# Optimization experiments

Measured on AMD Instinct MI355X. Metric: run time of the kernel, lower is better.

The kernel has to match this reference:

```python
import jax, jax.numpy as jnp
import numpy as np

N_HIDDEN = 32
RANK = 6
SV_DECAY_GAMMA = 0.3
LEAK_ALPHA = 0.1
INPUT_DIM = 64
OUTPUT_DIM = 32


def setup_inputs() -> dict:
    key = jax.random.key(0)
    ks = jax.random.split(key, 8)
    B, T = 256, 2048
    inputs = jax.random.normal(ks[0], (B, T, INPUT_DIM), dtype=jnp.float32)
    # parameters (match torch init scales)
    m = jax.random.normal(ks[1], (N_HIDDEN, 1), dtype=jnp.float32) * 0.1
    n = jax.random.normal(ks[2], (N_HIDDEN, 1), dtype=jnp.float32) * 0.1
    M = jax.random.normal(ks[3], (N_HIDDEN, RANK), dtype=jnp.float32) * 0.1
    Nmat = jax.random.normal(ks[4], (N_HIDDEN, RANK), dtype=jnp.float32) * 0.1
    # singular-value-decay scaling of M, N (as in _initialize_with_sv_decay)
    target_sv = jnp.exp(-SV_DECAY_GAMMA * jnp.arange(RANK, dtype=jnp.float32))
    target_sv = target_sv / target_sv.sum() * RANK
    sqrt_sv = jnp.sqrt(target_sv)
    M = M * sqrt_sv[None, :]
    Nmat = Nmat * sqrt_sv[None, :]
    bias = jnp.zeros((N_HIDDEN,), dtype=jnp.float32)
    # W_in: Linear(input_dim, N, bias=False) -> weight [N, input_dim]
    lim_in = 1.0 / np.sqrt(INPUT_DIM)
    W_in = jax.random.uniform(ks[5], (N_HIDDEN, INPUT_DIM), minval=-lim_in, maxval=lim_in, dtype=jnp.float32)
    lim_out = 1.0 / np.sqrt(N_HIDDEN)
    W_out = jax.random.uniform(ks[6], (OUTPUT_DIM, N_HIDDEN), minval=-lim_out, maxval=lim_out, dtype=jnp.float32)
    b_out = jax.random.uniform(ks[7], (OUTPUT_DIM,), minval=-lim_out, maxval=lim_out, dtype=jnp.float32)
    return {"inputs": inputs, "W_in": W_in, "m": m, "n": n, "M": M,
            "Nmat": Nmat, "bias": bias, "W_out": W_out, "b_out": b_out}


def reference(inputs, W_in, m, n, M, Nmat, bias, W_out, b_out):
    # h_{t+1} = (1-a) h_t + a * tanh(W_rec h_t + W_in u_t + b); y_t = W_out h_t + b_out
    B, T, _ = inputs.shape
    alpha = LEAK_ALPHA
    # W_rec = m n^T + M N^T (time-invariant; torch recomputes per step, same math)
    W_rec = m @ n.T + M @ Nmat.T                         # [N, N]
    x_proj = jnp.einsum('bti,ni->btn', inputs, W_in)     # [B, T, N]
    h0 = jnp.zeros((B, N_HIDDEN), dtype=inputs.dtype)

    def step(h, x_t):
        pre = h @ W_rec.T + x_t + bias
        h_new = (1.0 - alpha) * h + alpha * jnp.tanh(pre)
        return h_new, h_new

    h_final, hs = jax.lax.scan(step, h0, jnp.swapaxes(x_proj, 0, 1))  # hs: [T, B, N]
    outputs = jnp.einsum('tbn,on->bto', hs, W_out) + b_out            # [B, T, O]
    return outputs, h_final
```

## Files before the change

### kernel.cpp

```cpp
#include <hip/hip_runtime.h>

#define RNN_B 256
#define RNN_T 2048
#define RNN_IN 64
#define RNN_N 32
#define RNN_O 32
#define RNN_R 6
#define RNN_ALPHA 0.1f
#define KSCALE 2.8853900817779268f

__global__ __launch_bounds__(256) void k_xproj(
    const float* __restrict__ u, const float* __restrict__ W_in,
    const float* __restrict__ bias, float* __restrict__ xp)
{
    const int tid = blockIdx.x * 256 + threadIdx.x;
    const float4* __restrict__ u4 =
        reinterpret_cast<const float4*>(u) + (size_t)tid * (RNN_IN / 4);
    float acc[RNN_N];
    #pragma unroll
    for (int n = 0; n < RNN_N; ++n) acc[n] = bias[n];
    #pragma unroll
    for (int q = 0; q < RNN_IN / 4; ++q) {
        const float4 v = u4[q];
        #pragma unroll
        for (int n = 0; n < RNN_N; ++n) {
            const float* wr = W_in + n * RNN_IN + 4 * q;
            acc[n] = fmaf(wr[0], v.x, acc[n]);
            acc[n] = fmaf(wr[1], v.y, acc[n]);
            acc[n] = fmaf(wr[2], v.z, acc[n]);
            acc[n] = fmaf(wr[3], v.w, acc[n]);
        }
    }
    float4* __restrict__ o4 =
        reinterpret_cast<float4*>(xp) + (size_t)tid * (RNN_N / 4);
    #pragma unroll
    for (int q = 0; q < RNN_N / 4; ++q)
        o4[q] = make_float4(KSCALE * acc[4*q+0], KSCALE * acc[4*q+1],
                            KSCALE * acc[4*q+2], KSCALE * acc[4*q+3]);
}

template <int CTRL>
__device__ __forceinline__ float dpp_add(float v) {
    int t = __builtin_amdgcn_update_dpp(0, __float_as_int(v), CTRL, 0xf, 0xf, true);
    return v + __int_as_float(t);
}

__device__ __forceinline__ float xhalf_sum(float v) {
#if __has_builtin(__builtin_amdgcn_permlane32_swap)
    typedef int v2i __attribute__((ext_vector_type(2)));
    v2i r = __builtin_amdgcn_permlane32_swap(__float_as_int(v),
                                             __float_as_int(v), false, false);
    return __int_as_float(r.x) + __int_as_float(r.y);
#else
    return v + __shfl_xor(v, 32, 64);
#endif
}

__device__ __forceinline__ float fast_exp2(float x) {
#if __has_builtin(__builtin_amdgcn_exp2f)
    return __builtin_amdgcn_exp2f(x);
#else
    return __expf(x * 0.6931471805599453f);
#endif
}
__device__ __forceinline__ float fast_rcp(float x) {
#if __has_builtin(__builtin_amdgcn_rcpf)
    return __builtin_amdgcn_rcpf(x);
#else
    return __frcp_rn(x);
#endif
}

__global__ __launch_bounds__(64, 1) void k_recur(
    const float* __restrict__ m, const float* __restrict__ nvec,
    const float* __restrict__ Mmat, const float* __restrict__ Nmat,
    const float* __restrict__ xp,
    float* __restrict__ hout,
    float* __restrict__ hfin)
{
    const int b    = blockIdx.x;
    const int lane = threadIdx.x;
    const int k    = lane & 15;
    const int iA   = 2 * k;
    const int iB   = 2 * k + 1;
    const int half = (lane >> 5) & 1;

    float cnA[4], cnB[4], cmA[4], cmB[4];
    #pragma unroll
    for (int j = 0; j < 4; ++j) {
        const int r = 4 * half + j;
        if (r == 0) {
            cnA[j] = nvec[iA];              cnB[j] = nvec[iB];
            cmA[j] = KSCALE * m[iA];        cmB[j] = KSCALE * m[iB];
        } else if (r <= RNN_R) {
            cnA[j] = Nmat[iA*RNN_R + (r-1)];          cnB[j] = Nmat[iB*RNN_R + (r-1)];
            cmA[j] = KSCALE * Mmat[iA*RNN_R + (r-1)]; cmB[j] = KSCALE * Mmat[iB*RNN_R + (r-1)];
        } else {
            cnA[j] = 0.f; cnB[j] = 0.f; cmA[j] = 0.f; cmB[j] = 0.f;
        }
    }
    const float xmask = (half == 0) ? 1.0f : 0.0f;

    const float2* __restrict__ x2 =
        reinterpret_cast<const float2*>(xp + (size_t)b * (RNN_T * RNN_N)) + k;
    float2* __restrict__ h2 =
        reinterpret_cast<float2*>(hout + (size_t)b * (RNN_T * RNN_N));

    float hA = 0.0f, hB = 0.0f;

    const int PF = 8;
    float2 xr[PF];
    #pragma unroll
    for (int i = 0; i < PF; ++i) xr[i] = x2[i * (RNN_N / 2)];

    #pragma unroll 8
    for (int t = 0; t < RNN_T; ++t) {
        const float xA = xr[0].x, xB = xr[0].y;
        #pragma unroll
        for (int i = 0; i < PF - 1; ++i) xr[i] = xr[i + 1];
        xr[PF - 1] = x2[(t + PF) * (RNN_N / 2)];

        float s0 = fmaf(hB, cnB[0], hA * cnA[0]);
        float s1 = fmaf(hB, cnB[1], hA * cnA[1]);
        float s2 = fmaf(hB, cnB[2], hA * cnA[2]);
        float s3 = fmaf(hB, cnB[3], hA * cnA[3]);
        s0 = dpp_add<0xB1>(s0);  s1 = dpp_add<0xB1>(s1);
        s2 = dpp_add<0xB1>(s2);  s3 = dpp_add<0xB1>(s3);
        s0 = dpp_add<0x4E>(s0);  s1 = dpp_add<0x4E>(s1);
        s2 = dpp_add<0x4E>(s2);  s3 = dpp_add<0x4E>(s3);
        s0 = dpp_add<0x141>(s0); s1 = dpp_add<0x141>(s1);
        s2 = dpp_add<0x141>(s2); s3 = dpp_add<0x141>(s3);
        s0 = dpp_add<0x140>(s0); s1 = dpp_add<0x140>(s1);
        s2 = dpp_add<0x140>(s2); s3 = dpp_add<0x140>(s3);

        float tA = fmaf(cmA[0], s0, fmaf(cmA[1], s1, xA * xmask));
        float tB = fmaf(cmB[0], s0, fmaf(cmB[1], s1, xB * xmask));
        float uA = fmaf(cmA[2], s2, cmA[3] * s3);
        float uB = fmaf(cmB[2], s2, cmB[3] * s3);
        const float zA = xhalf_sum(tA + uA);
        const float zB = xhalf_sum(tB + uB);

        const float eA = fast_exp2(zA), eB = fast_exp2(zB);
        const float gA = fmaf(1.0f - RNN_ALPHA, hA, RNN_ALPHA);
        const float gB = fmaf(1.0f - RNN_ALPHA, hB, RNN_ALPHA);
        hA = fmaf(-2.0f * RNN_ALPHA, fast_rcp(eA + 1.0f), gA);
        hB = fmaf(-2.0f * RNN_ALPHA, fast_rcp(eB + 1.0f), gB);

        if (lane < 16) h2[t * (RNN_N / 2) + lane] = make_float2(hA, hB);
    }
    if (lane < 16)
        reinterpret_cast<float2*>(hfin + (size_t)b * RNN_N)[lane] =
            make_float2(hA, hB);
}

__global__ __launch_bounds__(256) void k_out(
    const float* __restrict__ W_out, const float* __restrict__ b_out,
    const float* __restrict__ hsrc, float* __restrict__ ydst)
{
    const int tid = blockIdx.x * 256 + threadIdx.x;
    const float4* __restrict__ p4 =
        reinterpret_cast<const float4*>(hsrc) + (size_t)tid * (RNN_N / 4);
    float4* __restrict__ q4 =
        reinterpret_cast<float4*>(ydst) + (size_t)tid * (RNN_N / 4);
    float y[RNN_O];
    #pragma unroll
    for (int o = 0; o < RNN_O; ++o) y[o] = b_out[o];
    #pragma unroll
    for (int q = 0; q < RNN_N / 4; ++q) {
        const float4 v = p4[q];
        #pragma unroll
        for (int o = 0; o < RNN_O; ++o) {
            const float* wr = W_out + o * RNN_N + 4 * q;
            y[o] = fmaf(wr[0], v.x, y[o]);
            y[o] = fmaf(wr[1], v.y, y[o]);
            y[o] = fmaf(wr[2], v.z, y[o]);
            y[o] = fmaf(wr[3], v.w, y[o]);
        }
    }
    #pragma unroll
    for (int q = 0; q < RNN_N / 4; ++q)
        q4[q] = make_float4(y[4*q+0], y[4*q+1], y[4*q+2], y[4*q+3]);
}

extern "C" void kernel_launch(void* const* d_in, const int* in_sizes, int n_in,
                              void* d_out, int out_size, void* d_ws, size_t ws_size,
                              hipStream_t stream)
{
    const float* u     = (const float*)d_in[0];
    const float* W_in  = (const float*)d_in[1];
    const float* m     = (const float*)d_in[2];
    const float* nvec  = (const float*)d_in[3];
    const float* Mmat  = (const float*)d_in[4];
    const float* Nmat  = (const float*)d_in[5];
    const float* bias  = (const float*)d_in[6];
    const float* W_out = (const float*)d_in[7];
    const float* b_out = (const float*)d_in[8];
    float* out = (float*)d_out;

    float* hfin = out + (size_t)RNN_B * RNN_T * RNN_N;

    const size_t hbytes = (size_t)RNN_B * RNN_T * RNN_N * sizeof(float);
    float* hbuf = (ws_size >= hbytes) ? (float*)d_ws : out;

    k_xproj<<<(RNN_B * RNN_T) / 256, 256, 0, stream>>>(u, W_in, bias, out);
    k_recur<<<RNN_B, 64, 0, stream>>>(m, nvec, Mmat, Nmat, out, hbuf, hfin);
    k_out  <<<(RNN_B * RNN_T) / 256, 256, 0, stream>>>(W_out, b_out, hbuf, out);
}
```

Baseline: 608.4 us.

## Remap recurrence lanes to one hidden element each with staged cross-lane reductions

Changes the recurrent kernel's lane mapping so that each lane owns a single hidden element instead of a pair. Lanes are split by element parity and by rank group. The rank projections are now reduced with DPP within 16 lanes, then a permlane32 swap, and the output contribution with a permlane16 swap. This halves the per-lane exp/rcp and FMA work, and the prefetch buffer becomes a rotating slot instead of a shifted array. The cost is an extra cross-lane swap stage on the serial per-timestep dependency chain, and stores become scalar.

```diff
diff --git a/kernel.cpp b/kernel.cpp
--- a/kernel.cpp
+++ b/kernel.cpp
@@ -44,8 +44,15 @@
     int t = __builtin_amdgcn_update_dpp(0, __float_as_int(v), CTRL, 0xf, 0xf, true);
     return v + __int_as_float(t);
 }
-
-__device__ __forceinline__ float xhalf_sum(float v) {
+__device__ __forceinline__ float sum16(float v) {
+    v = dpp_add<0xB1>(v);
+    v = dpp_add<0x4E>(v);
+    v = dpp_add<0x141>(v);
+    v = dpp_add<0x140>(v);
+    return v;
+}
+
+__device__ __forceinline__ float xsum32(float v) {
 #if __has_builtin(__builtin_amdgcn_permlane32_swap)
     typedef int v2i __attribute__((ext_vector_type(2)));
     v2i r = __builtin_amdgcn_permlane32_swap(__float_as_int(v),
@@ -53,6 +60,16 @@
     return __int_as_float(r.x) + __int_as_float(r.y);
 #else
     return v + __shfl_xor(v, 32, 64);
+#endif
+}
+__device__ __forceinline__ float xsum16(float v) {
+#if __has_builtin(__builtin_amdgcn_permlane16_swap)
+    typedef int v2i __attribute__((ext_vector_type(2)));
+    v2i r = __builtin_amdgcn_permlane16_swap(__float_as_int(v),
+                                             __float_as_int(v), false, false);
+    return __int_as_float(r.x) + __int_as_float(r.y);
+#else
+    return v + __shfl_xor(v, 16, 64);
 #endif
 }
 
@@ -81,49 +98,42 @@
     const int b    = blockIdx.x;
     const int lane = threadIdx.x;
     const int k    = lane & 15;
-    const int iA   = 2 * k;
-    const int iB   = 2 * k + 1;
-    const int half = (lane >> 5) & 1;
-
-    float cnA[4], cnB[4], cmA[4], cmB[4];
+    const int q    = (lane >> 4) & 1;
+    const int p    = lane >> 5;
+    const int e    = 2 * k + p;
+
+    float cn[4], cm[4];
     #pragma unroll
     for (int j = 0; j < 4; ++j) {
-        const int r = 4 * half + j;
-        if (r == 0) {
-            cnA[j] = nvec[iA];              cnB[j] = nvec[iB];
-            cmA[j] = KSCALE * m[iA];        cmB[j] = KSCALE * m[iB];
-        } else if (r <= RNN_R) {
-            cnA[j] = Nmat[iA*RNN_R + (r-1)];          cnB[j] = Nmat[iB*RNN_R + (r-1)];
-            cmA[j] = KSCALE * Mmat[iA*RNN_R + (r-1)]; cmB[j] = KSCALE * Mmat[iB*RNN_R + (r-1)];
-        } else {
-            cnA[j] = 0.f; cnB[j] = 0.f; cmA[j] = 0.f; cmB[j] = 0.f;
-        }
-    }
-    const float xmask = (half == 0) ? 1.0f : 0.0f;
+        const int r = 4 * q + j;
+        float cnv = 0.f, cmv = 0.f;
+        if (r == 0)      { cnv = nvec[e];              cmv = m[e]; }
+        else if (r <= RNN_R) { cnv = Nmat[e*RNN_R + (r-1)]; cmv = Mmat[e*RNN_R + (r-1)]; }
+        cn[j] = cnv;
+        cm[j] = KSCALE * cmv;
+    }
 
     const float2* __restrict__ x2 =
         reinterpret_cast<const float2*>(xp + (size_t)b * (RNN_T * RNN_N)) + k;
-    float2* __restrict__ h2 =
-        reinterpret_cast<float2*>(hout + (size_t)b * (RNN_T * RNN_N));
-
-    float hA = 0.0f, hB = 0.0f;
+    float* __restrict__ hbase = hout + (size_t)b * (RNN_T * RNN_N);
+
+    float h = 0.0f;
 
     const int PF = 8;
     float2 xr[PF];
     #pragma unroll
     for (int i = 0; i < PF; ++i) xr[i] = x2[i * (RNN_N / 2)];
 
+    const bool do_store = (q == 0);
+
     #pragma unroll 8
     for (int t = 0; t < RNN_T; ++t) {
-        const float xA = xr[0].x, xB = xr[0].y;
-        #pragma unroll
-        for (int i = 0; i < PF - 1; ++i) xr[i] = xr[i + 1];
-        xr[PF - 1] = x2[(t + PF) * (RNN_N / 2)];
-
-        float s0 = fmaf(hB, cnB[0], hA * cnA[0]);
-        float s1 = fmaf(hB, cnB[1], hA * cnA[1]);
-        float s2 = fmaf(hB, cnB[2], hA * cnA[2]);
-        float s3 = fmaf(hB, cnB[3], hA * cnA[3]);
+        const int slot = t & (PF - 1);
+        const float2 xv = xr[slot];
+        xr[slot] = x2[(t + PF) * (RNN_N / 2)];
+        const float xe = p ? xv.y : xv.x;
+
+        float s0 = cn[0] * h, s1 = cn[1] * h, s2 = cn[2] * h, s3 = cn[3] * h;
         s0 = dpp_add<0xB1>(s0);  s1 = dpp_add<0xB1>(s1);
         s2 = dpp_add<0xB1>(s2);  s3 = dpp_add<0xB1>(s3);
         s0 = dpp_add<0x4E>(s0);  s1 = dpp_add<0x4E>(s1);
@@ -133,24 +143,19 @@
         s0 = dpp_add<0x140>(s0); s1 = dpp_add<0x140>(s1);
         s2 = dpp_add<0x140>(s2); s3 = dpp_add<0x140>(s3);
 
-        float tA = fmaf(cmA[0], s0, fmaf(cmA[1], s1, xA * xmask));
-        float tB = fmaf(cmB[0], s0, fmaf(cmB[1], s1, xB * xmask));
-        float uA = fmaf(cmA[2], s2, cmA[3] * s3);
-        float uB = fmaf(cmB[2], s2, cmB[3] * s3);
-        const float zA = xhalf_sum(tA + uA);
-        const float zB = xhalf_sum(tB + uB);
-
-        const float eA = fast_exp2(zA), eB = fast_exp2(zB);
-        const float gA = fmaf(1.0f - RNN_ALPHA, hA, RNN_ALPHA);
-        const float gB = fmaf(1.0f - RNN_ALPHA, hB, RNN_ALPHA);
-        hA = fmaf(-2.0f * RNN_ALPHA, fast_rcp(eA + 1.0f), gA);
-        hB = fmaf(-2.0f * RNN_ALPHA, fast_rcp(eB + 1.0f), gB);
-
-        if (lane < 16) h2[t * (RNN_N / 2) + lane] = make_float2(hA, hB);
-    }
-    if (lane < 16)
-        reinterpret_cast<float2*>(hfin + (size_t)b * RNN_N)[lane] =
-            make_float2(hA, hB);
+        s0 = xsum32(s0); s1 = xsum32(s1); s2 = xsum32(s2); s3 = xsum32(s3);
+
+        float w = fmaf(cm[1], s1, cm[0] * s0) + fmaf(cm[3], s3, cm[2] * s2);
+        w = xsum16(w);
+        const float z = w + xe;
+
+        const float ez = fast_exp2(z);
+        const float g  = fmaf(1.0f - RNN_ALPHA, h, RNN_ALPHA);
+        h = fmaf(-2.0f * RNN_ALPHA, fast_rcp(ez + 1.0f), g);
+
+        if (do_store) hbase[t * RNN_N + e] = h;
+    }
+    if (do_store) hfin[b * RNN_N + e] = h;
 }
 
 __global__ __launch_bounds__(256) void k_out(
```

Result: slower. 620.9 us (+2.0%).
